# Optimization experiments

Hardware: AMD Instinct MI355X
Metric: run time of the kernel (lower is better)

The kernel has to match this reference:

```python
import jax, jax.numpy as jnp
import numpy as np

N, H, C, K, D = 16384, 16, 192, 43, 2
SIGMA = 1.0   # radius == sigma in Block
BN_EPS = 1e-5


def setup_inputs() -> dict:
    key = jax.random.key(0)
    ks = jax.random.split(key, 8)
    coord = jax.random.uniform(ks[0], (N, 3), dtype=jnp.float32)
    feat = jax.random.normal(ks[1], (N, C), dtype=jnp.float32)
    ref_idx = jax.random.randint(ks[2], (N, H), 0, N)
    # kernel point dispositions, within radius
    kp = jax.random.normal(ks[3], (K, 3), dtype=jnp.float32) * (0.3 * SIGMA)
    W1 = jax.random.normal(ks[4], (D, C, C), dtype=jnp.float32) / np.sqrt(C)
    Wk = jax.random.normal(ks[5], (D, K, C), dtype=jnp.float32) / np.sqrt(K * H)
    W3 = jax.random.normal(ks[6], (D, C, C), dtype=jnp.float32) / np.sqrt(C)
    ones = jnp.ones((D, C), jnp.float32)
    zeros = jnp.zeros((D, C), jnp.float32)
    return {
        "coord": coord, "feat": feat, "ref_idx": ref_idx, "kp": kp,
        "W1": W1, "Wk": Wk, "W3": W3,
        "g1": ones, "b1": zeros, "g2": ones, "b2": zeros, "g3": ones, "b3": zeros,
    }


def _bn(x, g, b):
    # PointBatchNorm on [N, C]: batch statistics over the point axis
    m = jnp.mean(x, axis=0)
    v = jnp.var(x, axis=0)
    return (x - m) * jax.lax.rsqrt(v + BN_EPS) * g + b


def reference(coord, feat, ref_idx, kp, W1, Wk, W3, g1, b1, g2, b2, g3, b3):
    # --- KP influence, shared across blocks (same coords / neighbor table) ---
    nb = coord[ref_idx] - coord[:, None, :]                       # [N,H,3] relative neighbor coords
    d2 = (jnp.sum(nb * nb, -1)[..., None]
          + jnp.sum(kp * kp, -1)[None, None, :]
          - 2.0 * jnp.einsum('nhd,kd->nhk', nb, kp))              # [N,H,K]
    d = jnp.sqrt(jnp.maximum(d2, 0.0))
    infl = jnp.maximum(1.0 - d / SIGMA, 0.0)                      # linear influence [N,H,K]

    relu = jax.nn.relu
    depth = W1.shape[0]
    for i in range(depth):
        identity = feat
        h = relu(_bn(feat @ W1[i], g1[i], b1[i]))                 # fc1 + BN + ReLU
        # KPConvD: depthwise kernel-point conv
        A = jnp.einsum('nhk,kc->nhc', infl, Wk[i])                # influence-projected depthwise weights
        h = jnp.einsum('nhc,nhc->nc', h[ref_idx], A)              # gather + weighted aggregate
        h = relu(_bn(h, g2[i], b2[i]))
        h = _bn(h @ W3[i], g3[i], b3[i])                          # fc3 + BN
        feat = relu(identity + h)                                 # skip + ReLU
    return feat
```

## Files before the change

### kernel.cpp

```cpp
#include <hip/hip_runtime.h>

#define N_PTS 16384
#define NH 16
#define NC 192
#define NK 43
#define ND 2
#define BN_EPS 1e-5f

typedef __attribute__((ext_vector_type(8))) short bf16x8;
typedef __attribute__((ext_vector_type(4))) float f32x4;

static __device__ __forceinline__ short f2bf(float f) {
    union { float f; unsigned u; } x; x.f = f;
    unsigned r = x.u + (0x7fffu + ((x.u >> 16) & 1u));
    return (short)(r >> 16);
}
static __device__ __forceinline__ float bf2f(short s) {
    union { unsigned u; float f; } x; x.u = ((unsigned)(unsigned short)s) << 16;
    return x.f;
}

__global__ __launch_bounds__(64) void k_wfrag(const float* __restrict__ W1,
                                              const float* __restrict__ Wk,
                                              const float* __restrict__ W3,
                                              short* __restrict__ Wb) {
    int b = blockIdx.x;
    int d = b / 168, r = b % 168;
    const float* src; short* dst; int kb, Ks, tile;
    if (r < 72)      { src = W1 + d * NC * NC; dst = Wb + d * 86016;         kb = 6; Ks = NC; tile = r; }
    else if (r < 96) { src = Wk + d * NK * NC; dst = Wb + d * 86016 + 36864; kb = 2; Ks = NK; tile = r - 72; }
    else             { src = W3 + d * NC * NC; dst = Wb + d * 86016 + 49152; kb = 6; Ks = NC; tile = r - 96; }
    int nt = tile / kb, ks = tile % kb;
    int lane = threadIdx.x, quad = lane >> 4, cl = lane & 15;
    bf16x8 vv;
#pragma unroll
    for (int j = 0; j < 8; ++j) {
        int k = ks * 32 + quad * 8 + j;
        vv[j] = (k < Ks) ? f2bf(src[k * NC + nt * 16 + cl]) : (short)0;
    }
    *(bf16x8*)(dst + ((nt * kb + ks) * 64 + lane) * 8) = vv;
}

__global__ __launch_bounds__(128) void k_stat2(const float* __restrict__ part, int nb,
                                               const float* __restrict__ g,
                                               const float* __restrict__ b,
                                               float* __restrict__ a_out,
                                               float* __restrict__ s_out) {
    __shared__ float red2[2];
    const int c = blockIdx.x;
    const int tid = threadIdx.x;
    const int lane = tid & 63;
    const int half = tid >> 6;
    const float* src = part + (half ? 192 + c : c);
    float s = 0.f;
    for (int i = lane; i < nb; i += 64) s += src[i * 384];
    s += __shfl_xor(s, 1);  s += __shfl_xor(s, 2);  s += __shfl_xor(s, 4);
    s += __shfl_xor(s, 8);  s += __shfl_xor(s, 16); s += __shfl_xor(s, 32);
    if (lane == 0) red2[half] = s;
    __syncthreads();
    if (tid == 0) {
        float m = red2[0] * (1.f / N_PTS);
        float var = red2[1] * (1.f / N_PTS) - m * m;
        float rs = rsqrtf(var + BN_EPS);
        float a = rs * g[c];
        a_out[c] = a;
        s_out[c] = b[c] - m * a;
    }
}

__global__ __launch_bounds__(192) void k_stat1b(const short* __restrict__ A,
                                                float* __restrict__ part) {
    __shared__ float red[8][384];
    const int tid = threadIdx.x;
    const int g = tid / 24, m = tid % 24;
    float s8[8], q8[8];
#pragma unroll
    for (int j = 0; j < 8; ++j) { s8[j] = 0.f; q8[j] = 0.f; }
#pragma unroll
    for (int p = 0; p < 4; ++p) {
        int row = blockIdx.x * 32 + p * 8 + g;
        bf16x8 v = *(const bf16x8*)(A + row * NC + m * 8);
#pragma unroll
        for (int j = 0; j < 8; ++j) {
            float x = bf2f(v[j]);
            s8[j] += x; q8[j] = fmaf(x, x, q8[j]);
        }
    }
#pragma unroll
    for (int j = 0; j < 8; ++j) {
        red[g][m * 8 + j] = s8[j];
        red[g][192 + m * 8 + j] = q8[j];
    }
    __syncthreads();
    float S = 0.f, Q = 0.f;
#pragma unroll
    for (int gg = 0; gg < 8; ++gg) { S += red[gg][tid]; Q += red[gg][192 + tid]; }
    part[blockIdx.x * 384 + tid] = S;
    part[blockIdx.x * 384 + 192 + tid] = Q;
}

__global__ __launch_bounds__(256) void k_gemm1(const float* __restrict__ feat,
                                               const short* __restrict__ T2prev,
                                               const float* __restrict__ st3prev,
                                               short* __restrict__ X1,
                                               const short* __restrict__ W1b,
                                               short* __restrict__ T,
                                               float* __restrict__ part) {
    __shared__ float red[4][384];
    const int tid = threadIdx.x;
    const int wave = tid >> 6, lane = tid & 63;
    const int quad = lane >> 4, cl = lane & 15;
    const int r0 = blockIdx.x * 64 + wave * 16;
    const int row = r0 + cl;

    f32x4 acc[12];
#pragma unroll
    for (int nt = 0; nt < 12; ++nt) acc[nt] = (f32x4){0.f, 0.f, 0.f, 0.f};

#pragma unroll
    for (int ks = 0; ks < 6; ++ks) {
        const int k0 = ks * 32 + quad * 8;
        const float* ap = feat + row * NC + k0;
        float4 a0 = *(const float4*)ap;
        float4 a1v = *(const float4*)(ap + 4);
        float x[8] = {a0.x, a0.y, a0.z, a0.w, a1v.x, a1v.y, a1v.z, a1v.w};
        if (T2prev) {
            bf16x8 t2 = *(const bf16x8*)(T2prev + row * NC + k0);
            float4 pa0 = *(const float4*)(st3prev + k0), pa1 = *(const float4*)(st3prev + k0 + 4);
            float4 ps0 = *(const float4*)(st3prev + 192 + k0), ps1 = *(const float4*)(st3prev + 192 + k0 + 4);
            float pav[8] = {pa0.x, pa0.y, pa0.z, pa0.w, pa1.x, pa1.y, pa1.z, pa1.w};
            float psv[8] = {ps0.x, ps0.y, ps0.z, ps0.w, ps1.x, ps1.y, ps1.z, ps1.w};
#pragma unroll
            for (int j = 0; j < 8; ++j)
                x[j] = fmaxf(x[j] + fmaf(pav[j], bf2f(t2[j]), psv[j]), 0.f);
        }
        bf16x8 af;
#pragma unroll
        for (int j = 0; j < 8; ++j) af[j] = f2bf(x[j]);
        if (T2prev) *(bf16x8*)(X1 + row * NC + k0) = af;
#pragma unroll
        for (int nt = 0; nt < 12; ++nt) {
            bf16x8 bf = *(const bf16x8*)(W1b + ((nt * 6 + ks) * 64 + lane) * 8);
            acc[nt] = __builtin_amdgcn_mfma_f32_16x16x32_bf16(af, bf, acc[nt], 0, 0, 0);
        }
    }
#pragma unroll
    for (int nt = 0; nt < 12; ++nt) {
        int c = nt * 16 + cl;
        float s = 0.f, sq = 0.f;
#pragma unroll
        for (int r = 0; r < 4; ++r) {
            float v = acc[nt][r];
            T[(r0 + quad * 4 + r) * NC + c] = f2bf(v);
            s += v; sq = fmaf(v, v, sq);
        }
        s += __shfl_xor(s, 16); s += __shfl_xor(s, 32);
        sq += __shfl_xor(sq, 16); sq += __shfl_xor(sq, 32);
        if (quad == 0) { red[wave][c] = s; red[wave][192 + c] = sq; }
    }
    __syncthreads();
    for (int t = tid; t < 384; t += 256)
        part[blockIdx.x * 384 + t] = red[0][t] + red[1][t] + red[2][t] + red[3][t];
}

__global__ __launch_bounds__(512) void k_kpconv(const float* __restrict__ coord,
                                                const int* __restrict__ ridx,
                                                const float* __restrict__ kp,
                                                const short* __restrict__ Wkb,
                                                const short* __restrict__ T,
                                                const float* __restrict__ st1,
                                                short* __restrict__ U) {
    __shared__ __align__(16) short wk_s[12288];
    __shared__ __align__(16) float4 kp_s[64];
    __shared__ float a1s[192], s1s[192];

    const int tid = threadIdx.x;
    {
        const float4* src = (const float4*)Wkb;
        float4* dst = (float4*)wk_s;
        for (int j = tid; j < 1536; j += 512) dst[j] = src[j];
        if (tid < 64) {
            bool ok = tid < NK;
            float x = ok ? kp[tid * 3 + 0] : 1e9f;
            float y = ok ? kp[tid * 3 + 1] : 1e9f;
            float z = ok ? kp[tid * 3 + 2] : 1e9f;
            kp_s[tid] = (float4){x, y, z, fmaf(x, x, fmaf(y, y, z * z))};
        }
        if (tid < 192) { a1s[tid] = st1[tid]; s1s[tid] = st1[192 + tid]; }
    }
    __syncthreads();

    const int wave = tid >> 6, lane = tid & 63;
    const int quad = lane >> 4, cl = lane & 15;
    const int n = blockIdx.x * 8 + wave;

    int idh = 0; float nbx = 0.f, nby = 0.f, nbz = 0.f;
    if (lane < NH) {
        idh = ridx[n * NH + lane];
        float cx = coord[n * 3 + 0], cy = coord[n * 3 + 1], cz = coord[n * 3 + 2];
        nbx = coord[idh * 3 + 0] - cx;
        nby = coord[idh * 3 + 1] - cy;
        nbz = coord[idh * 3 + 2] - cz;
    }
    const float nx = __shfl(nbx, cl), ny = __shfl(nby, cl), nz = __shfl(nbz, cl);
    int rowb[4];
#pragma unroll
    for (int r = 0; r < 4; ++r) rowb[r] = __shfl(idh, quad * 4 + r) * NC;

    unsigned short xv[12][4];
    const unsigned short* Tu = (const unsigned short*)T;
#pragma unroll
    for (int nt = 0; nt < 12; ++nt)
#pragma unroll
        for (int r = 0; r < 4; ++r)
            xv[nt][r] = Tu[rowb[r] + nt * 16 + cl];

    const float nb2 = fmaf(nx, nx, fmaf(ny, ny, nz * nz));
    const float m2x = -2.f * nx, m2y = -2.f * ny, m2z = -2.f * nz;
    bf16x8 af[2];
#pragma unroll
    for (int ks = 0; ks < 2; ++ks) {
#pragma unroll
        for (int j = 0; j < 8; ++j) {
            int k = ks * 32 + quad * 8 + j;
            float4 kpv = kp_s[k];
            float t = nb2 + kpv.w;
            t = fmaf(m2x, kpv.x, t);
            t = fmaf(m2y, kpv.y, t);
            t = fmaf(m2z, kpv.z, t);
            float d = sqrtf(fmaxf(t, 0.f));
            af[ks][j] = f2bf(fmaxf(1.f - d, 0.f));
        }
    }

    f32x4 acc[12];
#pragma unroll
    for (int nt = 0; nt < 12; ++nt) {
        bf16x8 b0 = *(const bf16x8*)(wk_s + ((nt * 2 + 0) * 64 + lane) * 8);
        bf16x8 b1v = *(const bf16x8*)(wk_s + ((nt * 2 + 1) * 64 + lane) * 8);
        f32x4 z = (f32x4){0.f, 0.f, 0.f, 0.f};
        z = __builtin_amdgcn_mfma_f32_16x16x32_bf16(af[0], b0, z, 0, 0, 0);
        acc[nt] = __builtin_amdgcn_mfma_f32_16x16x32_bf16(af[1], b1v, z, 0, 0, 0);
    }

#pragma unroll
    for (int nt = 0; nt < 12; ++nt) {
        const float a1c = a1s[nt * 16 + cl], s1c = s1s[nt * 16 + cl];
        float u = 0.f;
#pragma unroll
        for (int r = 0; r < 4; ++r) {
            float t = bf2f((short)xv[nt][r]);
            float x = fmaxf(fmaf(a1c, t, s1c), 0.f);
            u = fmaf(acc[nt][r], x, u);
        }
        u += __shfl_xor(u, 16);
        u += __shfl_xor(u, 32);
        if (quad == 0) U[n * NC + nt * 16 + cl] = f2bf(u);
    }
}

__global__ __launch_bounds__(256) void k_gemm3(const short* __restrict__ U,
                                               const float* __restrict__ st2,
                                               const short* __restrict__ W3b,
                                               short* __restrict__ T2,
                                               float* __restrict__ part) {
    __shared__ float red[4][384];
    const int tid = threadIdx.x;
    const int wave = tid >> 6, lane = tid & 63;
    const int quad = lane >> 4, cl = lane & 15;
    const int r0 = blockIdx.x * 64 + wave * 16;
    const int row = r0 + cl;

    f32x4 acc[12];
#pragma unroll
    for (int nt = 0; nt < 12; ++nt) acc[nt] = (f32x4){0.f, 0.f, 0.f, 0.f};

#pragma unroll
    for (int ks = 0; ks < 6; ++ks) {
        const int k0 = ks * 32 + quad * 8;
        bf16x8 u8 = *(const bf16x8*)(U + row * NC + k0);
        float4 aa0 = *(const float4*)(st2 + k0), aa1 = *(const float4*)(st2 + k0 + 4);
        float4 ss0 = *(const float4*)(st2 + 192 + k0), ss1 = *(const float4*)(st2 + 192 + k0 + 4);
        float av[8] = {aa0.x, aa0.y, aa0.z, aa0.w, aa1.x, aa1.y, aa1.z, aa1.w};
        float sv[8] = {ss0.x, ss0.y, ss0.z, ss0.w, ss1.x, ss1.y, ss1.z, ss1.w};
        bf16x8 af;
#pragma unroll
        for (int j = 0; j < 8; ++j)
            af[j] = f2bf(fmaxf(fmaf(av[j], bf2f(u8[j]), sv[j]), 0.f));
#pragma unroll
        for (int nt = 0; nt < 12; ++nt) {
            bf16x8 bf = *(const bf16x8*)(W3b + ((nt * 6 + ks) * 64 + lane) * 8);
            acc[nt] = __builtin_amdgcn_mfma_f32_16x16x32_bf16(af, bf, acc[nt], 0, 0, 0);
        }
    }
#pragma unroll
    for (int nt = 0; nt < 12; ++nt) {
        int c = nt * 16 + cl;
        float s = 0.f, sq = 0.f;
#pragma unroll
        for (int r = 0; r < 4; ++r) {
            float v = acc[nt][r];
            T2[(r0 + quad * 4 + r) * NC + c] = f2bf(v);
            s += v; sq = fmaf(v, v, sq);
        }
        s += __shfl_xor(s, 16); s += __shfl_xor(s, 32);
        sq += __shfl_xor(sq, 16); sq += __shfl_xor(sq, 32);
        if (quad == 0) { red[wave][c] = s; red[wave][192 + c] = sq; }
    }
    __syncthreads();
    for (int t = tid; t < 384; t += 256)
        part[blockIdx.x * 384 + t] = red[0][t] + red[1][t] + red[2][t] + red[3][t];
}

__global__ __launch_bounds__(256) void k_final(const short* __restrict__ T2,
                                               const float* __restrict__ st3,
                                               const short* __restrict__ X1,
                                               float* __restrict__ out) {
    const int i = blockIdx.x * 256 + threadIdx.x;
    const int c0 = (i * 8) % 192;
    bf16x8 t2 = *(const bf16x8*)(T2 + (long)i * 8);
    bf16x8 x1 = *(const bf16x8*)(X1 + (long)i * 8);
    float4 aa0 = *(const float4*)(st3 + c0), aa1 = *(const float4*)(st3 + c0 + 4);
    float4 ss0 = *(const float4*)(st3 + 192 + c0), ss1 = *(const float4*)(st3 + 192 + c0 + 4);
    float av[8] = {aa0.x, aa0.y, aa0.z, aa0.w, aa1.x, aa1.y, aa1.z, aa1.w};
    float sv[8] = {ss0.x, ss0.y, ss0.z, ss0.w, ss1.x, ss1.y, ss1.z, ss1.w};
    float4 o0, o1;
    float o[8];
#pragma unroll
    for (int j = 0; j < 8; ++j)
        o[j] = fmaxf(bf2f(x1[j]) + fmaf(av[j], bf2f(t2[j]), sv[j]), 0.f);
    o0 = (float4){o[0], o[1], o[2], o[3]};
    o1 = (float4){o[4], o[5], o[6], o[7]};
    *(float4*)(out + (long)i * 8)     = o0;
    *(float4*)(out + (long)i * 8 + 4) = o1;
}

extern "C" void kernel_launch(void* const* d_in, const int* in_sizes, int n_in,
                              void* d_out, int out_size, void* d_ws, size_t ws_size,
                              hipStream_t stream) {
    const float* coord = (const float*)d_in[0];
    const float* feat  = (const float*)d_in[1];
    const int*   ridx  = (const int*)d_in[2];
    const float* kp    = (const float*)d_in[3];
    const float* W1    = (const float*)d_in[4];
    const float* Wk    = (const float*)d_in[5];
    const float* W3    = (const float*)d_in[6];
    const float* g1    = (const float*)d_in[7];
    const float* b1    = (const float*)d_in[8];
    const float* g2    = (const float*)d_in[9];
    const float* b2    = (const float*)d_in[10];
    const float* g3    = (const float*)d_in[11];
    const float* b3    = (const float*)d_in[12];
    float* out = (float*)d_out;

    float* part  = (float*)d_ws;
    float* stats = part + 512 * 384;
    short* X1 = (short*)(stats + 2304);
    short* T  = X1 + N_PTS * NC;
    short* U  = T + N_PTS * NC;
    short* T2 = U + N_PTS * NC;
    short* Wb = T2 + N_PTS * NC;

    k_wfrag<<<336, 64, 0, stream>>>(W1, Wk, W3, Wb);

    for (int d = 0; d < ND; ++d) {
        const short* W1b = Wb + d * 86016;
        const short* Wkb = W1b + 36864;
        const short* W3b = W1b + 49152;
        float* st1 = stats + (d * 3 + 0) * 384;
        float* st2 = stats + (d * 3 + 1) * 384;
        float* st3 = stats + (d * 3 + 2) * 384;

        k_gemm1<<<256, 256, 0, stream>>>(feat,
                                         d ? T2 : (short*)nullptr,
                                         stats + 2 * 384,
                                         X1, W1b, T, part);
        k_stat2<<<192, 128, 0, stream>>>(part, 256, g1 + d * NC, b1 + d * NC, st1, st1 + 192);
        k_kpconv<<<N_PTS / 8, 512, 0, stream>>>(coord, ridx, kp, Wkb, T, st1, U);
        k_stat1b<<<512, 192, 0, stream>>>(U, part);
        k_stat2<<<192, 128, 0, stream>>>(part, 512, g2 + d * NC, b2 + d * NC, st2, st2 + 192);
        k_gemm3<<<256, 256, 0, stream>>>(U, st2, W3b, T2, part);
        k_stat2<<<192, 128, 0, stream>>>(part, 256, g3 + d * NC, b3 + d * NC, st3, st3 + 192);
    }
    k_final<<<N_PTS * NC / 8 / 256, 256, 0, stream>>>(T2, stats + 5 * 384, X1, out);
}
```

Measured before the change: 264.2 us.

## Fuse BN2 partial statistics into kpconv and transpose partials layout

Removes the separate k_stat1b pass that reread U, and has k_kpconv write per-block channel sums and sums of squares directly into a partials buffer. Partials are now stored channel-major (stride 2048), so k_stat2 reads contiguous entries instead of strided ones. This adds shared memory and a block sync to k_kpconv, which may reduce its occupancy. Statistics are now taken from the fp32 values before bf16 rounding, a small numerical change.

```diff
diff --git a/kernel.cpp b/kernel.cpp
--- a/kernel.cpp
+++ b/kernel.cpp
@@ -6,6 +6,7 @@
 #define NK 43
 #define ND 2
 #define BN_EPS 1e-5f
+#define PSTRIDE 2048
 
 typedef __attribute__((ext_vector_type(8))) short bf16x8;
 typedef __attribute__((ext_vector_type(4))) float f32x4;
@@ -51,9 +52,9 @@
     const int tid = threadIdx.x;
     const int lane = tid & 63;
     const int half = tid >> 6;
-    const float* src = part + (half ? 192 + c : c);
+    const float* src = part + (half ? (long)(192 + c) * PSTRIDE : (long)c * PSTRIDE);
     float s = 0.f;
-    for (int i = lane; i < nb; i += 64) s += src[i * 384];
+    for (int i = lane; i < nb; i += 64) s += src[i];
     s += __shfl_xor(s, 1);  s += __shfl_xor(s, 2);  s += __shfl_xor(s, 4);
     s += __shfl_xor(s, 8);  s += __shfl_xor(s, 16); s += __shfl_xor(s, 32);
     if (lane == 0) red2[half] = s;
@@ -66,37 +67,6 @@
         a_out[c] = a;
         s_out[c] = b[c] - m * a;
     }
-}
-
-__global__ __launch_bounds__(192) void k_stat1b(const short* __restrict__ A,
-                                                float* __restrict__ part) {
-    __shared__ float red[8][384];
-    const int tid = threadIdx.x;
-    const int g = tid / 24, m = tid % 24;
-    float s8[8], q8[8];
-#pragma unroll
-    for (int j = 0; j < 8; ++j) { s8[j] = 0.f; q8[j] = 0.f; }
-#pragma unroll
-    for (int p = 0; p < 4; ++p) {
-        int row = blockIdx.x * 32 + p * 8 + g;
-        bf16x8 v = *(const bf16x8*)(A + row * NC + m * 8);
-#pragma unroll
-        for (int j = 0; j < 8; ++j) {
-            float x = bf2f(v[j]);
-            s8[j] += x; q8[j] = fmaf(x, x, q8[j]);
-        }
-    }
-#pragma unroll
-    for (int j = 0; j < 8; ++j) {
-        red[g][m * 8 + j] = s8[j];
-        red[g][192 + m * 8 + j] = q8[j];
-    }
-    __syncthreads();
-    float S = 0.f, Q = 0.f;
-#pragma unroll
-    for (int gg = 0; gg < 8; ++gg) { S += red[gg][tid]; Q += red[gg][192 + tid]; }
-    part[blockIdx.x * 384 + tid] = S;
-    part[blockIdx.x * 384 + 192 + tid] = Q;
 }
 
 __global__ __launch_bounds__(256) void k_gemm1(const float* __restrict__ feat,
@@ -160,7 +130,7 @@
     }
     __syncthreads();
     for (int t = tid; t < 384; t += 256)
-        part[blockIdx.x * 384 + t] = red[0][t] + red[1][t] + red[2][t] + red[3][t];
+        part[(long)t * PSTRIDE + blockIdx.x] = red[0][t] + red[1][t] + red[2][t] + red[3][t];
 }
 
 __global__ __launch_bounds__(512) void k_kpconv(const float* __restrict__ coord,
@@ -169,10 +139,12 @@
                                                 const short* __restrict__ Wkb,
                                                 const short* __restrict__ T,
                                                 const float* __restrict__ st1,
-                                                short* __restrict__ U) {
+                                                short* __restrict__ U,
+                                                float* __restrict__ part) {
     __shared__ __align__(16) short wk_s[12288];
     __shared__ __align__(16) float4 kp_s[64];
     __shared__ float a1s[192], s1s[192];
+    __shared__ float red[8][384];
 
     const int tid = threadIdx.x;
     {
@@ -255,7 +227,17 @@
         }
         u += __shfl_xor(u, 16);
         u += __shfl_xor(u, 32);
-        if (quad == 0) U[n * NC + nt * 16 + cl] = f2bf(u);
+        if (quad == 0) {
+            U[n * NC + nt * 16 + cl] = f2bf(u);
+            red[wave][nt * 16 + cl] = u;
+            red[wave][192 + nt * 16 + cl] = u * u;
+        }
+    }
+    __syncthreads();
+    for (int t = tid; t < 384; t += 512) {
+        float S = red[0][t] + red[1][t] + red[2][t] + red[3][t]
+                + red[4][t] + red[5][t] + red[6][t] + red[7][t];
+        part[(long)t * PSTRIDE + blockIdx.x] = S;
     }
 }
 
@@ -309,7 +291,7 @@
     }
     __syncthreads();
     for (int t = tid; t < 384; t += 256)
-        part[blockIdx.x * 384 + t] = red[0][t] + red[1][t] + red[2][t] + red[3][t];
+        part[(long)t * PSTRIDE + blockIdx.x] = red[0][t] + red[1][t] + red[2][t] + red[3][t];
 }
 
 __global__ __launch_bounds__(256) void k_final(const short* __restrict__ T2,
@@ -324,15 +306,12 @@
     float4 ss0 = *(const float4*)(st3 + 192 + c0), ss1 = *(const float4*)(st3 + 192 + c0 + 4);
     float av[8] = {aa0.x, aa0.y, aa0.z, aa0.w, aa1.x, aa1.y, aa1.z, aa1.w};
     float sv[8] = {ss0.x, ss0.y, ss0.z, ss0.w, ss1.x, ss1.y, ss1.z, ss1.w};
-    float4 o0, o1;
     float o[8];
 #pragma unroll
     for (int j = 0; j < 8; ++j)
         o[j] = fmaxf(bf2f(x1[j]) + fmaf(av[j], bf2f(t2[j]), sv[j]), 0.f);
-    o0 = (float4){o[0], o[1], o[2], o[3]};
-    o1 = (float4){o[4], o[5], o[6], o[7]};
-    *(float4*)(out + (long)i * 8)     = o0;
-    *(float4*)(out + (long)i * 8 + 4) = o1;
+    *(float4*)(out + (long)i * 8)     = (float4){o[0], o[1], o[2], o[3]};
+    *(float4*)(out + (long)i * 8 + 4) = (float4){o[4], o[5], o[6], o[7]};
 }
 
 extern "C" void kernel_launch(void* const* d_in, const int* in_sizes, int n_in,
@@ -354,7 +333,7 @@
     float* out = (float*)d_out;
 
     float* part  = (float*)d_ws;
-    float* stats = part + 512 * 384;
+    float* stats = part + 384 * PSTRIDE;
     short* X1 = (short*)(stats + 2304);
     short* T  = X1 + N_PTS * NC;
     short* U  = T + N_PTS * NC;
@@ -376,9 +355,8 @@
                                          stats + 2 * 384,
                                          X1, W1b, T, part);
         k_stat2<<<192, 128, 0, stream>>>(part, 256, g1 + d * NC, b1 + d * NC, st1, st1 + 192);
-        k_kpconv<<<N_PTS / 8, 512, 0, stream>>>(coord, ridx, kp, Wkb, T, st1, U);
-        k_stat1b<<<512, 192, 0, stream>>>(U, part);
-        k_stat2<<<192, 128, 0, stream>>>(part, 512, g2 + d * NC, b2 + d * NC, st2, st2 + 192);
+        k_kpconv<<<N_PTS / 8, 512, 0, stream>>>(coord, ridx, kp, Wkb, T, st1, U, part);
+        k_stat2<<<192, 128, 0, stream>>>(part, 2048, g2 + d * NC, b2 + d * NC, st2, st2 + 192);
         k_gemm3<<<256, 256, 0, stream>>>(U, st2, W3b, T2, part);
         k_stat2<<<192, 128, 0, stream>>>(part, 256, g3 + d * NC, b3 + d * NC, st3, st3 + 192);
     }
```

Result: slower. 281.6 us (+6.6%).
